# Kernel optimization log

Measured on AMD Instinct MI355X. Metric: run time of the kernel, lower is better.

The kernel has to match this reference:

```python
import jax, jax.numpy as jnp
import numpy as np

B, A, N, G, F = 16, 256, 64, 64, 128  # batch, atoms, neighbors, gaussians, filters
CUTOFF = 5.0


def ssp(x):
    # shifted softplus: ln(0.5*e^x + 0.5)
    return jax.nn.softplus(x) - jnp.log(2.0).astype(x.dtype)


def setup_inputs() -> dict:
    key = jax.random.key(0)
    ks = jax.random.split(key, 10)
    x = jax.random.normal(ks[0], (B, A, F), jnp.float32)
    r_ij = jax.random.uniform(ks[1], (B, A, N), jnp.float32) * 6.0  # some beyond cutoff
    f_ij = jax.random.uniform(ks[2], (B, A, N, G), jnp.float32)  # gaussian-expanded dists
    neighbors = jax.random.randint(ks[3], (B, A, N), 0, A)
    pairwise_mask = (jax.random.uniform(ks[4], (B, A, N)) < 0.9).astype(jnp.float32)
    s = lambda fan: 1.0 / np.sqrt(fan)
    fw1 = jax.random.normal(ks[5], (G, F), jnp.float32) * s(G)
    fb1 = jnp.zeros((F,), jnp.float32)
    fw2 = jax.random.normal(ks[6], (F, F), jnp.float32) * s(F)
    fb2 = jnp.zeros((F,), jnp.float32)
    w_in2f = jax.random.normal(ks[7], (F, F), jnp.float32) * s(F)
    w_f2out = jax.random.normal(ks[8], (F, F), jnp.float32) * s(F)
    b_f2out = jnp.zeros((F,), jnp.float32)
    return {"x": x, "r_ij": r_ij, "f_ij": f_ij, "neighbors": neighbors,
            "pairwise_mask": pairwise_mask, "fw1": fw1, "fb1": fb1, "fw2": fw2,
            "fb2": fb2, "w_in2f": w_in2f, "w_f2out": w_f2out, "b_f2out": b_f2out}


def reference(x, r_ij, f_ij, neighbors, pairwise_mask,
              fw1, fb1, fw2, fb2, w_in2f, w_f2out, b_f2out):
    # filter network: Dense(G->F, ssp) -> Dense(F->F)
    W = ssp(jnp.einsum('bang,gf->banf', f_ij, fw1) + fb1)
    W = jnp.einsum('banf,fh->banh', W, fw2) + fb2  # [B,A,N,F]
    # cosine cutoff
    C = 0.5 * (jnp.cos(r_ij * (jnp.pi / CUTOFF)) + 1.0)
    C = C * (r_ij < CUTOFF).astype(r_ij.dtype)
    W = W * C[..., None]
    # in2f (no bias), then gather neighbor features along atom axis
    y = jnp.einsum('bad,df->baf', x, w_in2f)  # [B,A,F]
    bidx = jnp.arange(y.shape[0])[:, None, None]
    y_nbh = y[bidx, neighbors]  # [B,A,N,F]
    # filter-weight multiply + masked sum aggregate over neighbor axis
    y = jnp.sum(y_nbh * W * pairwise_mask[..., None], axis=2)  # [B,A,F]
    # f2out with shifted-softplus activation
    return ssp(jnp.einsum('baf,fo->bao', y, w_f2out) + b_f2out)
```

## Files before the change

kernel.cpp:

```cpp
#include <hip/hip_runtime.h>
#include <hip/hip_bf16.h>
#include <math.h>

#define B_ 16
#define A_ 256
#define N_ 64
#define G_ 64
#define F_ 128
#define APB 8

typedef __attribute__((ext_vector_type(8))) short short8;
typedef __attribute__((ext_vector_type(4))) float floatx4;

__device__ __forceinline__ float ssp(float x) {
    const float t = __expf(-fabsf(x));
    return fmaxf(x, 0.0f) + __logf(1.0f + t) - 0.69314718055994531f;
}
__device__ __forceinline__ unsigned f2bf(float f) {
    union { float f; unsigned u; } v; v.f = f;
    v.u += 0x7fffu + ((v.u >> 16) & 1u);
    return v.u >> 16;
}
__device__ __forceinline__ float bf2f_lo(unsigned d) {
    union { unsigned i; float f; } v; v.i = d << 16; return v.f;
}
__device__ __forceinline__ float bf2f_hi(unsigned d) {
    union { unsigned i; float f; } v; v.i = d & 0xffff0000u; return v.f;
}
__device__ __forceinline__ short8 pack_bf8(const float4& v0, const float4& v1) {
    short8 t;
    t[0] = (short)f2bf(v0.x); t[1] = (short)f2bf(v0.y);
    t[2] = (short)f2bf(v0.z); t[3] = (short)f2bf(v0.w);
    t[4] = (short)f2bf(v1.x); t[5] = (short)f2bf(v1.y);
    t[6] = (short)f2bf(v1.z); t[7] = (short)f2bf(v1.w);
    return t;
}

__global__ __launch_bounds__(256) void k0_repack(
    const float* __restrict__ fw1, const float* __restrict__ fw2,
    const float* __restrict__ win, const float* __restrict__ wout,
    unsigned short* __restrict__ fw1B, unsigned short* __restrict__ fw2B,
    unsigned short* __restrict__ winB, unsigned short* __restrict__ woutB)
{
    int idx = blockIdx.x * 1024 + threadIdx.x * 4;
    #pragma unroll
    for (int u = 0; u < 4; ++u, ++idx) {
        if (idx < 8192) {
            const int j  = idx & 7;
            const int l  = (idx >> 3) & 63;
            const int ks = (idx >> 9) & 1;
            const int tf = idx >> 10;
            const int g  = ks * 32 + (l >> 4) * 8 + j;
            const int f  = tf * 16 + (l & 15);
            fw1B[idx] = (unsigned short)f2bf(fw1[g * F_ + f]);
        } else {
            const int i2  = (idx - 8192) & 16383;
            const int sel = (idx - 8192) >> 14;
            const int j  = i2 & 7;
            const int l  = (i2 >> 3) & 63;
            const int ks = (i2 >> 9) & 3;
            const int tf = i2 >> 11;
            const int k  = ks * 32 + (l >> 4) * 8 + j;
            const int f  = tf * 16 + (l & 15);
            const float v = (sel == 0) ? fw2[k * F_ + f]
                          : (sel == 1) ? win[k * F_ + f]
                                       : wout[k * F_ + f];
            unsigned short* dst = (sel == 0) ? fw2B : (sel == 1) ? winB : woutB;
            dst[i2] = (unsigned short)f2bf(v);
        }
    }
}

__global__ __launch_bounds__(256) void in2f_gemm(
    const float* __restrict__ x, const unsigned short* __restrict__ winB,
    unsigned short* __restrict__ ypre)
{
    const int tid = threadIdx.x;
    const int w = tid >> 6, l = tid & 63, quad = l >> 4, c0 = l & 15;
    const int row = blockIdx.x * 64 + w * 16 + c0;

    short8 a[4];
    {
        const float* base = x + (size_t)row * F_ + quad * 8;
        #pragma unroll
        for (int ks = 0; ks < 4; ++ks)
            a[ks] = pack_bf8(*(const float4*)(base + ks * 32),
                             *(const float4*)(base + ks * 32 + 4));
    }

    const short8* W8 = (const short8*)winB;
    floatx4 acc[8];
    #pragma unroll
    for (int tf = 0; tf < 8; ++tf) acc[tf] = (floatx4){0.f,0.f,0.f,0.f};
    #pragma unroll
    for (int ks = 0; ks < 4; ++ks)
        #pragma unroll
        for (int tf = 0; tf < 8; ++tf)
            acc[tf] = __builtin_amdgcn_mfma_f32_16x16x32_bf16(
                a[ks], W8[(tf * 4 + ks) * 64 + l], acc[tf], 0, 0, 0);

    #pragma unroll
    for (int r = 0; r < 4; ++r) {
        const int ro = blockIdx.x * 64 + w * 16 + quad * 4 + r;
        short8 s;
        #pragma unroll
        for (int tf = 0; tf < 8; ++tf) s[tf] = (short)f2bf(acc[tf][r]);
        *(short8*)&ypre[(size_t)ro * F_ + c0 * 8] = s;
    }
}

__global__ __launch_bounds__(512) void cfconv_kernel(
    const float* __restrict__ r_ij, const float* __restrict__ f_ij,
    const int*   __restrict__ nbrs, const float* __restrict__ mask,
    const float* __restrict__ fb1,  const float* __restrict__ fb2,
    const unsigned short* __restrict__ ypre,
    const unsigned short* __restrict__ fw1B,
    const unsigned short* __restrict__ fw2B,
    unsigned short* __restrict__ y_agg)
{
    __shared__ unsigned short s_w[24576];
    __shared__ short s_h1[N_ * F_];
    __shared__ float s_scale[2][N_];
    __shared__ int   s_nb[2][N_];
    __shared__ float s_red[4][F_];

    const int tid  = threadIdx.x;
    const int w    = tid >> 6;
    const int l    = tid & 63;
    const int quad = l >> 4;
    const int c0   = l & 15;
    const int rw   = w & 3;
    const int h    = w >> 2;

    const int abase = blockIdx.x * APB;
    const int b     = abase >> 8;

    {
        const uint4* w1 = (const uint4*)fw1B;
        const uint4* w2 = (const uint4*)fw2B;
        uint4* dst = (uint4*)s_w;
        #pragma unroll
        for (int i = 0; i < 6; ++i) {
            const int idx = tid + i * 512;
            dst[idx] = (idx < 1024) ? w1[idx] : w2[idx - 1024];
        }
    }
    if (h == 0 && l < 16) {
        const int n = rw * 16 + l;
        const float r = r_ij[(size_t)abase * N_ + n];
        const float c = (r < 5.0f)
            ? 0.5f * (__cosf(r * 0.62831853071795865f) + 1.0f)
            : 0.0f;
        s_scale[0][n] = c * mask[(size_t)abase * N_ + n];
        s_nb[0][n]    = nbrs[(size_t)abase * N_ + n];
    }
    float4 pf[4];
    {
        const float* base = f_ij + (size_t)abase * (N_ * G_)
                          + (size_t)(rw * 16 + c0) * G_ + quad * 8;
        pf[0] = *(const float4*)(base);
        pf[1] = *(const float4*)(base + 4);
        pf[2] = *(const float4*)(base + 32);
        pf[3] = *(const float4*)(base + 36);
    }
    float fb1v[4], fb2v[4];
    #pragma unroll
    for (int t = 0; t < 4; ++t) {
        fb1v[t] = fb1[(h * 4 + t) * 16 + c0];
        fb2v[t] = fb2[(h * 4 + t) * 16 + c0];
    }
    __syncthreads();

    const short8* sw1 = (const short8*)s_w;
    const short8* sw2 = (const short8*)(s_w + 8192);
    const unsigned short* yb = ypre + (size_t)b * A_ * F_;

    for (int i = 0; i < APB; ++i) {
        const int atom = abase + i;
        const int buf  = i & 1;

        short8 a1[2];
        a1[0] = pack_bf8(pf[0], pf[1]);
        a1[1] = pack_bf8(pf[2], pf[3]);

        floatx4 acc1[4];
        #pragma unroll
        for (int t = 0; t < 4; ++t) acc1[t] = (floatx4){0.f,0.f,0.f,0.f};
        #pragma unroll
        for (int ks = 0; ks < 2; ++ks)
            #pragma unroll
            for (int t = 0; t < 4; ++t) {
                const int tf = h * 4 + t;
                acc1[t] = __builtin_amdgcn_mfma_f32_16x16x32_bf16(
                    a1[ks], sw1[(tf * 2 + ks) * 64 + l], acc1[t], 0, 0, 0);
            }

        if (i + 1 < APB) {
            const float* base = f_ij + (size_t)(atom + 1) * (N_ * G_)
                              + (size_t)(rw * 16 + c0) * G_ + quad * 8;
            pf[0] = *(const float4*)(base);
            pf[1] = *(const float4*)(base + 4);
            pf[2] = *(const float4*)(base + 32);
            pf[3] = *(const float4*)(base + 36);
            if (h == 0 && l < 16) {
                const int n = rw * 16 + l;
                const float r = r_ij[(size_t)(atom + 1) * N_ + n];
                const float c = (r < 5.0f)
                    ? 0.5f * (__cosf(r * 0.62831853071795865f) + 1.0f)
                    : 0.0f;
                s_scale[buf ^ 1][n] = c * mask[(size_t)(atom + 1) * N_ + n];
                s_nb[buf ^ 1][n]    = nbrs[(size_t)(atom + 1) * N_ + n];
            }
        }

        #pragma unroll
        for (int t = 0; t < 4; ++t) {
            const int   tf    = h * 4 + t;
            const int   chunk = tf * 2 + (c0 >> 3);
            const int   o     = c0 & 7;
            #pragma unroll
            for (int r = 0; r < 4; ++r) {
                const int row_l = quad * 4 + r;
                const float v = ssp(acc1[t][r] + fb1v[t]);
                s_h1[(rw * 16 + row_l) * F_ + ((chunk ^ row_l) * 8) + o] =
                    (short)f2bf(v);
            }
        }
        __syncthreads();

        short8 a2[4];
        #pragma unroll
        for (int ks = 0; ks < 4; ++ks)
            a2[ks] = *(const short8*)&s_h1[(rw * 16 + c0) * F_
                                           + (((ks * 4 + quad) ^ c0) * 8)];

        float scl[4];
        uint2 yv[4];
        #pragma unroll
        for (int r = 0; r < 4; ++r) {
            const int n = rw * 16 + quad * 4 + r;
            scl[r] = s_scale[buf][n];
            yv[r] = *(const uint2*)&yb[(size_t)s_nb[buf][n] * F_
                                       + c0 * 8 + h * 4];
        }

        floatx4 acc2[4];
        #pragma unroll
        for (int t = 0; t < 4; ++t) acc2[t] = (floatx4){0.f,0.f,0.f,0.f};
        #pragma unroll
        for (int ks = 0; ks < 4; ++ks)
            #pragma unroll
            for (int t = 0; t < 4; ++t) {
                const int tf = h * 4 + t;
                acc2[t] = __builtin_amdgcn_mfma_f32_16x16x32_bf16(
                    a2[ks], sw2[(tf * 4 + ks) * 64 + l], acc2[t], 0, 0, 0);
            }

        float part[4];
        #pragma unroll
        for (int t = 0; t < 4; ++t) part[t] = 0.0f;
        #pragma unroll
        for (int r = 0; r < 4; ++r) {
            const unsigned d0 = yv[r].x, d1 = yv[r].y;
            part[0] = fmaf((acc2[0][r] + fb2v[0]) * scl[r], bf2f_lo(d0), part[0]);
            part[1] = fmaf((acc2[1][r] + fb2v[1]) * scl[r], bf2f_hi(d0), part[1]);
            part[2] = fmaf((acc2[2][r] + fb2v[2]) * scl[r], bf2f_lo(d1), part[2]);
            part[3] = fmaf((acc2[3][r] + fb2v[3]) * scl[r], bf2f_hi(d1), part[3]);
        }
        #pragma unroll
        for (int t = 0; t < 4; ++t) {
            part[t] += __shfl_xor(part[t], 16, 64);
            part[t] += __shfl_xor(part[t], 32, 64);
        }
        if (l < 16) {
            #pragma unroll
            for (int t = 0; t < 4; ++t)
                s_red[rw][(h * 4 + t) * 16 + l] = part[t];
        }
        __syncthreads();

        if (tid < F_) {
            const float v = s_red[0][tid] + s_red[1][tid]
                          + s_red[2][tid] + s_red[3][tid];
            y_agg[(size_t)atom * F_ + tid] = (unsigned short)f2bf(v);
        }
    }
}

__global__ __launch_bounds__(256) void f2out_kernel(
    const unsigned short* __restrict__ y_agg,
    const unsigned short* __restrict__ woutB,
    const float* __restrict__ bias, float* __restrict__ out)
{
    const int tid = threadIdx.x;
    const int w = tid >> 6, l = tid & 63, quad = l >> 4, c0 = l & 15;
    const int row = blockIdx.x * 64 + w * 16 + c0;

    short8 a[4];
    #pragma unroll
    for (int ks = 0; ks < 4; ++ks)
        a[ks] = *(const short8*)&y_agg[(size_t)row * F_ + ks * 32 + quad * 8];

    const short8* W8 = (const short8*)woutB;
    floatx4 acc[8];
    #pragma unroll
    for (int tf = 0; tf < 8; ++tf) acc[tf] = (floatx4){0.f,0.f,0.f,0.f};
    #pragma unroll
    for (int ks = 0; ks < 4; ++ks)
        #pragma unroll
        for (int tf = 0; tf < 8; ++tf)
            acc[tf] = __builtin_amdgcn_mfma_f32_16x16x32_bf16(
                a[ks], W8[(tf * 4 + ks) * 64 + l], acc[tf], 0, 0, 0);

    #pragma unroll
    for (int tf = 0; tf < 8; ++tf) {
        const float bs = bias[tf * 16 + c0];
        #pragma unroll
        for (int r = 0; r < 4; ++r) {
            const int ro = blockIdx.x * 64 + w * 16 + quad * 4 + r;
            out[(size_t)ro * F_ + tf * 16 + c0] = ssp(acc[tf][r] + bs);
        }
    }
}

extern "C" void kernel_launch(void* const* d_in, const int* in_sizes, int n_in,
                              void* d_out, int out_size, void* d_ws, size_t ws_size,
                              hipStream_t stream) {
    const float* x        = (const float*)d_in[0];
    const float* r_ij     = (const float*)d_in[1];
    const float* f_ij     = (const float*)d_in[2];
    const int*   nbrs     = (const int*)  d_in[3];
    const float* mask     = (const float*)d_in[4];
    const float* fw1      = (const float*)d_in[5];
    const float* fb1      = (const float*)d_in[6];
    const float* fw2      = (const float*)d_in[7];
    const float* fb2      = (const float*)d_in[8];
    const float* w_in2f   = (const float*)d_in[9];
    const float* w_f2out  = (const float*)d_in[10];
    const float* b_f2out  = (const float*)d_in[11];
    float* out = (float*)d_out;

    unsigned short* ypre  = (unsigned short*)d_ws;
    unsigned short* fw1B  = ypre  + (size_t)B_ * A_ * F_;
    unsigned short* fw2B  = fw1B  + 8192;
    unsigned short* winB  = fw2B  + 16384;
    unsigned short* woutB = winB  + 16384;
    unsigned short* y_agg = woutB + 16384;

    k0_repack<<<56, 256, 0, stream>>>(
        fw1, fw2, w_in2f, w_f2out, fw1B, fw2B, winB, woutB);
    in2f_gemm<<<B_ * A_ / 64, 256, 0, stream>>>(x, winB, ypre);
    cfconv_kernel<<<B_ * A_ / APB, 512, 0, stream>>>(
        r_ij, f_ij, nbrs, mask, fb1, fb2, ypre, fw1B, fw2B, y_agg);
    f2out_kernel<<<B_ * A_ / 64, 256, 0, stream>>>(y_agg, woutB, b_f2out, out);
}
```

Before: 156.7 us.

## Prefetch neighbor features one atom ahead, fold biases into MFMA init, faster ssp

Moves the gathered neighbor-feature and scale loads for the next atom ahead of the current atom's second GEMM, using register double-buffering so the global gather latency overlaps with MFMA work. Biases are now used as the MFMA accumulator's initial value instead of being added afterwards, and the first GEMM is issued after the next f_ij prefetch. ssp now uses native exp2/log builtins. The cost is extra registers for the prefetched data, which could lower occupancy.

Measured after the change: 165.8 us. +5.8%, slower.

```diff
diff --git a/kernel.cpp b/kernel.cpp
--- a/kernel.cpp
+++ b/kernel.cpp
@@ -13,8 +13,14 @@
 typedef __attribute__((ext_vector_type(4))) float floatx4;
 
 __device__ __forceinline__ float ssp(float x) {
+#if __has_builtin(__builtin_amdgcn_exp2f) && __has_builtin(__builtin_amdgcn_logf)
+    const float t = __builtin_amdgcn_exp2f(-1.44269504089f * fabsf(x));
+    const float l = __builtin_amdgcn_logf(1.0f + t);
+    return fmaf(0.69314718055994531f, l - 1.0f, fmaxf(x, 0.0f));
+#else
     const float t = __expf(-fabsf(x));
     return fmaxf(x, 0.0f) + __logf(1.0f + t) - 0.69314718055994531f;
+#endif
 }
 __device__ __forceinline__ unsigned f2bf(float f) {
     union { float f; unsigned u; } v; v.f = f;
@@ -175,6 +181,15 @@
     const short8* sw2 = (const short8*)(s_w + 8192);
     const unsigned short* yb = ypre + (size_t)b * A_ * F_;
 
+    float scl[4];
+    uint2 yv[4];
+    #pragma unroll
+    for (int r = 0; r < 4; ++r) {
+        const int n = rw * 16 + quad * 4 + r;
+        scl[r] = s_scale[0][n];
+        yv[r]  = *(const uint2*)&yb[(size_t)s_nb[0][n] * F_ + c0 * 8 + h * 4];
+    }
+
     for (int i = 0; i < APB; ++i) {
         const int atom = abase + i;
         const int buf  = i & 1;
@@ -182,18 +197,6 @@
         short8 a1[2];
         a1[0] = pack_bf8(pf[0], pf[1]);
         a1[1] = pack_bf8(pf[2], pf[3]);
-
-        floatx4 acc1[4];
-        #pragma unroll
-        for (int t = 0; t < 4; ++t) acc1[t] = (floatx4){0.f,0.f,0.f,0.f};
-        #pragma unroll
-        for (int ks = 0; ks < 2; ++ks)
-            #pragma unroll
-            for (int t = 0; t < 4; ++t) {
-                const int tf = h * 4 + t;
-                acc1[t] = __builtin_amdgcn_mfma_f32_16x16x32_bf16(
-                    a1[ks], sw1[(tf * 2 + ks) * 64 + l], acc1[t], 0, 0, 0);
-            }
 
         if (i + 1 < APB) {
             const float* base = f_ij + (size_t)(atom + 1) * (N_ * G_)
@@ -213,6 +216,19 @@
             }
         }
 
+        floatx4 acc1[4];
+        #pragma unroll
+        for (int t = 0; t < 4; ++t)
+            acc1[t] = (floatx4){fb1v[t], fb1v[t], fb1v[t], fb1v[t]};
+        #pragma unroll
+        for (int ks = 0; ks < 2; ++ks)
+            #pragma unroll
+            for (int t = 0; t < 4; ++t) {
+                const int tf = h * 4 + t;
+                acc1[t] = __builtin_amdgcn_mfma_f32_16x16x32_bf16(
+                    a1[ks], sw1[(tf * 2 + ks) * 64 + l], acc1[t], 0, 0, 0);
+            }
+
         #pragma unroll
         for (int t = 0; t < 4; ++t) {
             const int   tf    = h * 4 + t;
@@ -221,7 +237,7 @@
             #pragma unroll
             for (int r = 0; r < 4; ++r) {
                 const int row_l = quad * 4 + r;
-                const float v = ssp(acc1[t][r] + fb1v[t]);
+                const float v = ssp(acc1[t][r]);
                 s_h1[(rw * 16 + row_l) * F_ + ((chunk ^ row_l) * 8) + o] =
                     (short)f2bf(v);
             }
@@ -234,19 +250,22 @@
             a2[ks] = *(const short8*)&s_h1[(rw * 16 + c0) * F_
                                            + (((ks * 4 + quad) ^ c0) * 8)];
 
-        float scl[4];
-        uint2 yv[4];
-        #pragma unroll
-        for (int r = 0; r < 4; ++r) {
-            const int n = rw * 16 + quad * 4 + r;
-            scl[r] = s_scale[buf][n];
-            yv[r] = *(const uint2*)&yb[(size_t)s_nb[buf][n] * F_
-                                       + c0 * 8 + h * 4];
+        float scl_n[4];
+        uint2 yv_n[4];
+        if (i + 1 < APB) {
+            #pragma unroll
+            for (int r = 0; r < 4; ++r) {
+                const int n = rw * 16 + quad * 4 + r;
+                scl_n[r] = s_scale[buf ^ 1][n];
+                yv_n[r]  = *(const uint2*)&yb[(size_t)s_nb[buf ^ 1][n] * F_
+                                              + c0 * 8 + h * 4];
+            }
         }
 
         floatx4 acc2[4];
         #pragma unroll
-        for (int t = 0; t < 4; ++t) acc2[t] = (floatx4){0.f,0.f,0.f,0.f};
+        for (int t = 0; t < 4; ++t)
+            acc2[t] = (floatx4){fb2v[t], fb2v[t], fb2v[t], fb2v[t]};
         #pragma unroll
         for (int ks = 0; ks < 4; ++ks)
             #pragma unroll
@@ -262,10 +281,10 @@
         #pragma unroll
         for (int r = 0; r < 4; ++r) {
             const unsigned d0 = yv[r].x, d1 = yv[r].y;
-            part[0] = fmaf((acc2[0][r] + fb2v[0]) * scl[r], bf2f_lo(d0), part[0]);
-            part[1] = fmaf((acc2[1][r] + fb2v[1]) * scl[r], bf2f_hi(d0), part[1]);
-            part[2] = fmaf((acc2[2][r] + fb2v[2]) * scl[r], bf2f_lo(d1), part[2]);
-            part[3] = fmaf((acc2[3][r] + fb2v[3]) * scl[r], bf2f_hi(d1), part[3]);
+            part[0] = fmaf(acc2[0][r] * scl[r], bf2f_lo(d0), part[0]);
+            part[1] = fmaf(acc2[1][r] * scl[r], bf2f_hi(d0), part[1]);
+            part[2] = fmaf(acc2[2][r] * scl[r], bf2f_lo(d1), part[2]);
+            part[3] = fmaf(acc2[3][r] * scl[r], bf2f_hi(d1), part[3]);
         }
         #pragma unroll
         for (int t = 0; t < 4; ++t) {
@@ -284,6 +303,9 @@
                           + s_red[2][tid] + s_red[3][tid];
             y_agg[(size_t)atom * F_ + tid] = (unsigned short)f2bf(v);
         }
+
+        #pragma unroll
+        for (int r = 0; r < 4; ++r) { scl[r] = scl_n[r]; yv[r] = yv_n[r]; }
     }
 }
 
@@ -304,7 +326,10 @@
     const short8* W8 = (const short8*)woutB;
     floatx4 acc[8];
     #pragma unroll
-    for (int tf = 0; tf < 8; ++tf) acc[tf] = (floatx4){0.f,0.f,0.f,0.f};
+    for (int tf = 0; tf < 8; ++tf) {
+        const float bs = bias[tf * 16 + c0];
+        acc[tf] = (floatx4){bs, bs, bs, bs};
+    }
     #pragma unroll
     for (int ks = 0; ks < 4; ++ks)
         #pragma unroll
@@ -314,11 +339,10 @@
 
     #pragma unroll
     for (int tf = 0; tf < 8; ++tf) {
-        const float bs = bias[tf * 16 + c0];
         #pragma unroll
         for (int r = 0; r < 4; ++r) {
             const int ro = blockIdx.x * 64 + w * 16 + quad * 4 + r;
-            out[(size_t)ro * F_ + tf * 16 + c0] = ssp(acc[tf][r] + bs);
+            out[(size_t)ro * F_ + tf * 16 + c0] = ssp(acc[tf][r]);
         }
     }
 }
```
